# Kernel optimization log

Measured on AMD Instinct MI355X. Metric: run time of the kernel, lower is better.

## Reference

```python
import jax, jax.numpy as jnp
import numpy as np

N = 100000
E = 1600000
D_IN = 128
HID = 128
LN_EPS = 1e-5
GIN_EPS = 0.0  # PyG GINConv default eps


def setup_inputs() -> dict:
    key = jax.random.key(0)
    ks = jax.random.split(key, 8)
    x = jax.random.normal(ks[0], (N, D_IN), dtype=jnp.float32)
    edge_index = jax.random.randint(ks[1], (2, E), 0, N, dtype=jnp.int64)
    s1 = 1.0 / np.sqrt(D_IN)
    s2 = 1.0 / np.sqrt(HID)
    W1 = jax.random.uniform(ks[2], (D_IN, HID), jnp.float32, -s1, s1)
    b1 = jnp.zeros((HID,), jnp.float32)
    W2 = jax.random.uniform(ks[3], (HID, HID), jnp.float32, -s2, s2)
    b2 = jnp.zeros((HID,), jnp.float32)
    gamma = jnp.ones((HID,), jnp.float32)
    beta = jnp.zeros((HID,), jnp.float32)
    Wres = jax.random.uniform(ks[4], (D_IN, HID), jnp.float32, -s1, s1)
    bres = jnp.zeros((HID,), jnp.float32)
    return {"x": x, "edge_index": edge_index, "W1": W1, "b1": b1,
            "W2": W2, "b2": b2, "gamma": gamma, "beta": beta,
            "Wres": Wres, "bres": bres}


def reference(x, edge_index, W1, b1, W2, b2, gamma, beta, Wres, bres):
    src, dst = edge_index[0], edge_index[1]
    # GIN sum aggregation: scatter-add source features onto targets. [N, D_IN]
    agg = jax.ops.segment_sum(x[src], dst, num_segments=N)
    h = (1.0 + GIN_EPS) * x + agg
    # GIN MLP: Linear -> ReLU -> Linear
    h = jax.nn.relu(h @ W1 + b1) @ W2 + b2
    # LayerNorm over hidden dim
    mu = jnp.mean(h, axis=-1, keepdims=True)
    var = jnp.mean(jnp.square(h - mu), axis=-1, keepdims=True)
    h = (h - mu) * jax.lax.rsqrt(var + LN_EPS) * gamma + beta
    # dropout p=0 is identity; residual linear path
    return h + (x @ Wres + bres)
```

## Files before the change

### kernel.cpp

```cpp
#include <hip/hip_runtime.h>

#define NN 100000
#define NE 1600000
#define D 128
#define RT 64
#define NB 196
#define CAP 9216
#define PADB 136
#define TS 16
#define CVB 2048
#define BKB 391

typedef unsigned short u16;
typedef __attribute__((ext_vector_type(8))) short bf16x8;
typedef __attribute__((ext_vector_type(4))) float f32x4;

__device__ __forceinline__ u16 f2bf(float f) {
  unsigned int u = __float_as_uint(f);
  u += 0x7fffu + ((u >> 16) & 1u);
  return (u16)(u >> 16);
}

__global__ __launch_bounds__(256) void prep_convert(
    const float* __restrict__ x,
    const float* __restrict__ W1, const float* __restrict__ W2,
    const float* __restrict__ Wres,
    u16* __restrict__ xh, u16* __restrict__ wt) {
  int b = blockIdx.x;
  int t = threadIdx.x;
  if (b < CVB) {
    for (int q = b * 256 + t; q < 3200000; q += CVB * 256) {
      float4 v = ((const float4*)x)[q];
      uint2 pk;
      pk.x = (unsigned)f2bf(v.x) | ((unsigned)f2bf(v.y) << 16);
      pk.y = (unsigned)f2bf(v.z) | ((unsigned)f2bf(v.w) << 16);
      ((uint2*)xh)[q] = pk;
    }
  } else {
    const float* W = (b == CVB) ? Wres : (b == CVB + 1) ? W1 : W2;
    u16* dst = wt + (size_t)(b - CVB) * 16384;
    for (int i = t; i < 16384; i += 256) {
      int n = i >> 7, k = i & 127;
      dst[i] = f2bf(W[k * 128 + n]);
    }
  }
}

__global__ __launch_bounds__(256) void bucket_kernel(const int* __restrict__ ei,
                                                     int* __restrict__ tail,
                                                     unsigned* __restrict__ buf) {
  __shared__ int lhist[NB], lbase[NB];
  int t = threadIdx.x;
  size_t e0 = (size_t)blockIdx.x * 4096;
  int s_[16], d_[16];
  for (int j = t; j < NB; j += 256) lhist[j] = 0;
  __syncthreads();
#pragma unroll
  for (int k = 0; k < 16; ++k) {
    size_t e = e0 + t + (size_t)k * 256;
    if (e < NE) {
      d_[k] = ei[NE + e];
      s_[k] = ei[e];
      atomicAdd(&lhist[d_[k] >> 9], 1);
    } else {
      d_[k] = -1;
    }
  }
  __syncthreads();
  for (int j = t; j < NB; j += 256) {
    int c = lhist[j];
    lbase[j] = c ? atomicAdd(&tail[j * TS], c) : 0;
    lhist[j] = 0;
  }
  __syncthreads();
#pragma unroll
  for (int k = 0; k < 16; ++k) {
    if (d_[k] >= 0) {
      int bk = d_[k] >> 9;
      int r = lbase[bk] + atomicAdd(&lhist[bk], 1);
      if (r < CAP)
        buf[(size_t)bk * CAP + r] = (unsigned)s_[k] | ((unsigned)(d_[k] & 511) << 17);
    }
  }
}

__global__ __launch_bounds__(512) void build_csr(const unsigned* __restrict__ buf,
                                                 const int* __restrict__ tail,
                                                 int* __restrict__ cnt,
                                                 int* __restrict__ start,
                                                 int* __restrict__ csr) {
  __shared__ int lhist[512], lpre[512], lsum[64];
  int b = blockIdx.x, t = threadIdx.x;
  int nE = tail[b * TS];
  if (nE > CAP) nE = CAP;
  size_t bBase = (size_t)b * CAP;
  lhist[t] = 0;
  __syncthreads();
  for (int i = t; i < nE; i += 512)
    atomicAdd(&lhist[buf[bBase + i] >> 17], 1);
  __syncthreads();
  if (t < 64) {
    int s = 0;
#pragma unroll
    for (int k = 0; k < 8; ++k) { int v = lhist[t * 8 + k]; lpre[t * 8 + k] = s; s += v; }
    lsum[t] = s;
  }
  __syncthreads();
  if (t == 0) {
    int s = 0;
    for (int k = 0; k < 64; ++k) { int v = lsum[k]; lsum[k] = s; s += v; }
  }
  __syncthreads();
  if (t < 64) {
    int o = lsum[t];
#pragma unroll
    for (int k = 0; k < 8; ++k) lpre[t * 8 + k] += o;
  }
  __syncthreads();
  int node = (b << 9) + t;
  if (node < NN) {
    cnt[node] = lhist[t];
    start[node] = (int)bBase + lpre[t];
  }
  lhist[t] = 0;
  __syncthreads();
  for (int i = t; i < nE; i += 512) {
    unsigned e = buf[bBase + i];
    int dl = e >> 17;
    int r = atomicAdd(&lhist[dl], 1);
    csr[bBase + lpre[dl] + r] = (int)(e & 0x1FFFFu);
  }
}

#define BFACC8(aL, aH, v)                                  \
  { aL.x += __uint_as_float((v).x << 16);                  \
    aL.y += __uint_as_float((v).x & 0xffff0000u);          \
    aL.z += __uint_as_float((v).y << 16);                  \
    aL.w += __uint_as_float((v).y & 0xffff0000u);          \
    aH.x += __uint_as_float((v).z << 16);                  \
    aH.y += __uint_as_float((v).z & 0xffff0000u);          \
    aH.z += __uint_as_float((v).w << 16);                  \
    aH.w += __uint_as_float((v).w & 0xffff0000u); }

__global__ __launch_bounds__(256, 6) void gather_kernel(const float* __restrict__ x,
                                                        const u16* __restrict__ xh,
                                                        const int* __restrict__ cnt,
                                                        const int* __restrict__ start,
                                                        const int* __restrict__ csr,
                                                        u16* __restrict__ h0h) {
  int g = blockIdx.x * 16 + (threadIdx.x >> 4);
  if (g >= NN) return;
  int lane = threadIdx.x & 15;
  int fo = lane * 8;
  int n = cnt[g];
  const int* sp = csr + start[g];

  float4 aL0 = make_float4(0.f, 0.f, 0.f, 0.f);
  float4 aH0 = aL0, aL1 = aL0, aH1 = aL0;

  int nfull = n & ~3;
  if (nfull > 0) {
    int s0 = sp[0], s1 = sp[1], s2 = sp[2], s3 = sp[3];
    uint4 v0 = *(const uint4*)&xh[(size_t)s0 * D + fo];
    uint4 v1 = *(const uint4*)&xh[(size_t)s1 * D + fo];
    uint4 v2 = *(const uint4*)&xh[(size_t)s2 * D + fo];
    uint4 v3 = *(const uint4*)&xh[(size_t)s3 * D + fo];
#pragma unroll 2
    for (int j = 4; j < nfull; j += 4) {
      int t0 = sp[j], t1 = sp[j + 1], t2 = sp[j + 2], t3 = sp[j + 3];
      uint4 w0 = *(const uint4*)&xh[(size_t)t0 * D + fo];
      uint4 w1 = *(const uint4*)&xh[(size_t)t1 * D + fo];
      uint4 w2 = *(const uint4*)&xh[(size_t)t2 * D + fo];
      uint4 w3 = *(const uint4*)&xh[(size_t)t3 * D + fo];
      BFACC8(aL0, aH0, v0); BFACC8(aL1, aH1, v1);
      BFACC8(aL0, aH0, v2); BFACC8(aL1, aH1, v3);
      v0 = w0; v1 = w1; v2 = w2; v3 = w3;
    }
    BFACC8(aL0, aH0, v0); BFACC8(aL1, aH1, v1);
    BFACC8(aL0, aH0, v2); BFACC8(aL1, aH1, v3);
  }
  for (int j = nfull; j < n; ++j) {
    uint4 v0 = *(const uint4*)&xh[(size_t)sp[j] * D + fo];
    BFACC8(aL0, aH0, v0);
  }

  const float* xp = &x[(size_t)g * D + fo];
  float4 x0 = *(const float4*)xp;
  float4 x1 = *(const float4*)(xp + 4);
  float h0 = x0.x + aL0.x + aL1.x;
  float h1 = x0.y + aL0.y + aL1.y;
  float h2 = x0.z + aL0.z + aL1.z;
  float h3 = x0.w + aL0.w + aL1.w;
  float h4 = x1.x + aH0.x + aH1.x;
  float h5 = x1.y + aH0.y + aH1.y;
  float h6 = x1.z + aH0.z + aH1.z;
  float h7 = x1.w + aH0.w + aH1.w;
  uint4 pk;
  pk.x = (unsigned)f2bf(h0) | ((unsigned)f2bf(h1) << 16);
  pk.y = (unsigned)f2bf(h2) | ((unsigned)f2bf(h3) << 16);
  pk.z = (unsigned)f2bf(h4) | ((unsigned)f2bf(h5) << 16);
  pk.w = (unsigned)f2bf(h6) | ((unsigned)f2bf(h7) << 16);
  *(uint4*)&h0h[(size_t)g * 256 + fo] = pk;
}

__global__ __launch_bounds__(256, 3) void fused_kernel(
    const u16* __restrict__ xh, const u16* __restrict__ h0h,
    const u16* __restrict__ wt,
    const float* __restrict__ b1, const float* __restrict__ b2,
    const float* __restrict__ gamma, const float* __restrict__ beta,
    const float* __restrict__ bres, float* __restrict__ out) {
  __shared__ u16 Ws[128 * PADB];
  __shared__ u16 Hs[RT * PADB];

  const int t = threadIdx.x;
  const int w = t >> 6;
  const int lane = t & 63;
  const int quad = lane >> 4;
  const int l16 = lane & 15;
  const int row0 = blockIdx.x * RT;

  auto stageW = [&](const u16* __restrict__ src) {
#pragma unroll
    for (int i = 0; i < 16; ++i) {
      int v = t + i * 256;
      int r = v >> 5;
      int c4 = (v & 31) << 2;
      *(uint2*)&Ws[r * PADB + c4] = *(const uint2*)&src[r * D + c4];
    }
  };

  f32x4 acc[8], accR[8];
  f32x4 zz = {0.f, 0.f, 0.f, 0.f};
#pragma unroll
  for (int i = 0; i < 8; ++i) { acc[i] = zz; accR[i] = zz; }

  auto gemmGA = [&](const u16* __restrict__ Ag, int astride, f32x4 (&dd)[8]) {
    bf16x8 af[4];
    int ar = row0 + w * 16 + l16;
    if (ar > NN - 1) ar = NN - 1;
#pragma unroll
    for (int s = 0; s < 4; ++s)
      af[s] = *(const bf16x8*)&Ag[(size_t)ar * astride + s * 32 + quad * 8];
#pragma unroll
    for (int nt = 0; nt < 8; ++nt) {
      const u16* wp = &Ws[(nt * 16 + l16) * PADB + quad * 8];
#pragma unroll
      for (int s = 0; s < 4; ++s) {
        bf16x8 bf = *(const bf16x8*)&wp[s * 32];
        dd[nt] = __builtin_amdgcn_mfma_f32_16x16x32_bf16(af[s], bf, dd[nt], 0, 0, 0);
      }
    }
  };
  auto gemmLA = [&](f32x4 (&dd)[8]) {
    bf16x8 af[4];
#pragma unroll
    for (int s = 0; s < 4; ++s)
      af[s] = *(const bf16x8*)&Hs[(w * 16 + l16) * PADB + s * 32 + quad * 8];
#pragma unroll
    for (int nt = 0; nt < 8; ++nt) {
      const u16* wp = &Ws[(nt * 16 + l16) * PADB + quad * 8];
#pragma unroll
      for (int s = 0; s < 4; ++s) {
        bf16x8 bf = *(const bf16x8*)&wp[s * 32];
        dd[nt] = __builtin_amdgcn_mfma_f32_16x16x32_bf16(af[s], bf, dd[nt], 0, 0, 0);
      }
    }
  };

  stageW(wt);
  __syncthreads();
  gemmGA(xh, D, accR);
  __syncthreads();
  stageW(wt + 16384);
  __syncthreads();
  gemmGA(h0h, 256, acc);
  __syncthreads();

#pragma unroll
  for (int nt = 0; nt < 8; ++nt) {
    int col = nt * 16 + l16;
    float bb = b1[col];
#pragma unroll
    for (int r = 0; r < 4; ++r) {
      float hv = acc[nt][r] + bb;
      hv = hv > 0.f ? hv : 0.f;
      Hs[(w * 16 + quad * 4 + r) * PADB + col] = f2bf(hv);
      acc[nt][r] = 0.f;
    }
  }
  stageW(wt + 32768);
  __syncthreads();
  gemmLA(acc);

  float b2v[8], gv[8], bev[8], brv[8];
#pragma unroll
  for (int nt = 0; nt < 8; ++nt) {
    int col = nt * 16 + l16;
    b2v[nt] = b2[col];
    gv[nt] = gamma[col];
    bev[nt] = beta[col];
    brv[nt] = bres[col];
  }
#pragma unroll
  for (int r = 0; r < 4; ++r) {
    float s = 0.f, s2 = 0.f;
#pragma unroll
    for (int nt = 0; nt < 8; ++nt) {
      float h = acc[nt][r] + b2v[nt];
      s += h;
      s2 += h * h;
    }
    for (int m = 1; m <= 8; m <<= 1) {
      s += __shfl_xor(s, m);
      s2 += __shfl_xor(s2, m);
    }
    float mu = s * 0.0078125f;
    float var = s2 * 0.0078125f - mu * mu;
    float rs = rsqrtf(var + 1e-5f);
    int row = row0 + w * 16 + quad * 4 + r;
    if (row < NN) {
#pragma unroll
      for (int nt = 0; nt < 8; ++nt) {
        float h = acc[nt][r] + b2v[nt];
        out[(size_t)row * D + nt * 16 + l16] =
            (h - mu) * rs * gv[nt] + bev[nt] + accR[nt][r] + brv[nt];
      }
    }
  }
}

extern "C" void kernel_launch(void* const* d_in, const int* in_sizes, int n_in,
                              void* d_out, int out_size, void* d_ws, size_t ws_size,
                              hipStream_t stream) {
  const float* x     = (const float*)d_in[0];
  const int*   ei    = (const int*)d_in[1];
  const float* W1    = (const float*)d_in[2];
  const float* b1    = (const float*)d_in[3];
  const float* W2    = (const float*)d_in[4];
  const float* b2    = (const float*)d_in[5];
  const float* gamma = (const float*)d_in[6];
  const float* beta  = (const float*)d_in[7];
  const float* Wres  = (const float*)d_in[8];
  const float* bres  = (const float*)d_in[9];
  float* out = (float*)d_out;

  int*      tail  = (int*)d_ws;
  unsigned* buf   = (unsigned*)(tail + NB * TS);
  int*      cnt   = (int*)(buf + (size_t)NB * CAP);
  int*      start = cnt + NN;
  int*      csr   = start + NN;
  u16*      xh    = (u16*)(csr + (size_t)NB * CAP);
  u16*      wt    = xh + (size_t)NN * D;

  u16* h0h = (u16*)out;

  hipMemsetAsync(tail, 0, NB * TS * sizeof(int), stream);
  prep_convert<<<CVB + 3, 256, 0, stream>>>(x, W1, W2, Wres, xh, wt);
  bucket_kernel<<<BKB, 256, 0, stream>>>(ei, tail, buf);
  build_csr<<<NB, 512, 0, stream>>>(buf, tail, cnt, start, csr);
  gather_kernel<<<(NN + 15) / 16, 256, 0, stream>>>(x, xh, cnt, start, csr, h0h);
  fused_kernel<<<(NN + RT - 1) / RT, 256, 0, stream>>>(
      xh, h0h, wt, b1, b2, gamma, beta, bres, out);
}
```

Before: 257.9 us.

## Fuse neighbor gather into fused GEMM kernel, staging aggregated rows in LDS

Removes the separate gather kernel and performs the CSR neighbor aggregation inside the fused MLP kernel, writing the bf16 h0 tile directly into shared memory instead of a global scratch buffer. This eliminates a kernel launch and the global write/read of the aggregated feature matrix. The Wres weight staging is issued before the gather to overlap with it. The risk is that the latency-bound random gather now runs at the lower occupancy of the LDS-heavy GEMM kernel.

```diff
diff --git a/kernel.cpp b/kernel.cpp
--- a/kernel.cpp
+++ b/kernel.cpp
@@ -142,70 +142,10 @@
     aH.z += __uint_as_float((v).w << 16);                  \
     aH.w += __uint_as_float((v).w & 0xffff0000u); }
 
-__global__ __launch_bounds__(256, 6) void gather_kernel(const float* __restrict__ x,
-                                                        const u16* __restrict__ xh,
-                                                        const int* __restrict__ cnt,
-                                                        const int* __restrict__ start,
-                                                        const int* __restrict__ csr,
-                                                        u16* __restrict__ h0h) {
-  int g = blockIdx.x * 16 + (threadIdx.x >> 4);
-  if (g >= NN) return;
-  int lane = threadIdx.x & 15;
-  int fo = lane * 8;
-  int n = cnt[g];
-  const int* sp = csr + start[g];
-
-  float4 aL0 = make_float4(0.f, 0.f, 0.f, 0.f);
-  float4 aH0 = aL0, aL1 = aL0, aH1 = aL0;
-
-  int nfull = n & ~3;
-  if (nfull > 0) {
-    int s0 = sp[0], s1 = sp[1], s2 = sp[2], s3 = sp[3];
-    uint4 v0 = *(const uint4*)&xh[(size_t)s0 * D + fo];
-    uint4 v1 = *(const uint4*)&xh[(size_t)s1 * D + fo];
-    uint4 v2 = *(const uint4*)&xh[(size_t)s2 * D + fo];
-    uint4 v3 = *(const uint4*)&xh[(size_t)s3 * D + fo];
-#pragma unroll 2
-    for (int j = 4; j < nfull; j += 4) {
-      int t0 = sp[j], t1 = sp[j + 1], t2 = sp[j + 2], t3 = sp[j + 3];
-      uint4 w0 = *(const uint4*)&xh[(size_t)t0 * D + fo];
-      uint4 w1 = *(const uint4*)&xh[(size_t)t1 * D + fo];
-      uint4 w2 = *(const uint4*)&xh[(size_t)t2 * D + fo];
-      uint4 w3 = *(const uint4*)&xh[(size_t)t3 * D + fo];
-      BFACC8(aL0, aH0, v0); BFACC8(aL1, aH1, v1);
-      BFACC8(aL0, aH0, v2); BFACC8(aL1, aH1, v3);
-      v0 = w0; v1 = w1; v2 = w2; v3 = w3;
-    }
-    BFACC8(aL0, aH0, v0); BFACC8(aL1, aH1, v1);
-    BFACC8(aL0, aH0, v2); BFACC8(aL1, aH1, v3);
-  }
-  for (int j = nfull; j < n; ++j) {
-    uint4 v0 = *(const uint4*)&xh[(size_t)sp[j] * D + fo];
-    BFACC8(aL0, aH0, v0);
-  }
-
-  const float* xp = &x[(size_t)g * D + fo];
-  float4 x0 = *(const float4*)xp;
-  float4 x1 = *(const float4*)(xp + 4);
-  float h0 = x0.x + aL0.x + aL1.x;
-  float h1 = x0.y + aL0.y + aL1.y;
-  float h2 = x0.z + aL0.z + aL1.z;
-  float h3 = x0.w + aL0.w + aL1.w;
-  float h4 = x1.x + aH0.x + aH1.x;
-  float h5 = x1.y + aH0.y + aH1.y;
-  float h6 = x1.z + aH0.z + aH1.z;
-  float h7 = x1.w + aH0.w + aH1.w;
-  uint4 pk;
-  pk.x = (unsigned)f2bf(h0) | ((unsigned)f2bf(h1) << 16);
-  pk.y = (unsigned)f2bf(h2) | ((unsigned)f2bf(h3) << 16);
-  pk.z = (unsigned)f2bf(h4) | ((unsigned)f2bf(h5) << 16);
-  pk.w = (unsigned)f2bf(h6) | ((unsigned)f2bf(h7) << 16);
-  *(uint4*)&h0h[(size_t)g * 256 + fo] = pk;
-}
-
 __global__ __launch_bounds__(256, 3) void fused_kernel(
-    const u16* __restrict__ xh, const u16* __restrict__ h0h,
-    const u16* __restrict__ wt,
+    const float* __restrict__ x, const u16* __restrict__ xh,
+    const int* __restrict__ cnt, const int* __restrict__ start,
+    const int* __restrict__ csr, const u16* __restrict__ wt,
     const float* __restrict__ b1, const float* __restrict__ b2,
     const float* __restrict__ gamma, const float* __restrict__ beta,
     const float* __restrict__ bres, float* __restrict__ out) {
@@ -229,18 +169,78 @@
     }
   };
 
+  stageW(wt);
+
+  {
+    const int grp = t >> 4;
+    const int gl = t & 15;
+    const int fo = gl * 8;
+    for (int pass = 0; pass < 4; ++pass) {
+      int r = pass * 16 + grp;
+      int g = row0 + r;
+      uint4 pk = make_uint4(0u, 0u, 0u, 0u);
+      if (g < NN) {
+        int n = cnt[g];
+        const int* sp = csr + start[g];
+        float4 aL0 = make_float4(0.f, 0.f, 0.f, 0.f);
+        float4 aH0 = aL0, aL1 = aL0, aH1 = aL0;
+        int nfull = n & ~3;
+        if (nfull > 0) {
+          int s0 = sp[0], s1 = sp[1], s2 = sp[2], s3 = sp[3];
+          uint4 v0 = *(const uint4*)&xh[(size_t)s0 * D + fo];
+          uint4 v1 = *(const uint4*)&xh[(size_t)s1 * D + fo];
+          uint4 v2 = *(const uint4*)&xh[(size_t)s2 * D + fo];
+          uint4 v3 = *(const uint4*)&xh[(size_t)s3 * D + fo];
+#pragma unroll 2
+          for (int j = 4; j < nfull; j += 4) {
+            int t0 = sp[j], t1 = sp[j + 1], t2 = sp[j + 2], t3 = sp[j + 3];
+            uint4 w0 = *(const uint4*)&xh[(size_t)t0 * D + fo];
+            uint4 w1 = *(const uint4*)&xh[(size_t)t1 * D + fo];
+            uint4 w2 = *(const uint4*)&xh[(size_t)t2 * D + fo];
+            uint4 w3 = *(const uint4*)&xh[(size_t)t3 * D + fo];
+            BFACC8(aL0, aH0, v0); BFACC8(aL1, aH1, v1);
+            BFACC8(aL0, aH0, v2); BFACC8(aL1, aH1, v3);
+            v0 = w0; v1 = w1; v2 = w2; v3 = w3;
+          }
+          BFACC8(aL0, aH0, v0); BFACC8(aL1, aH1, v1);
+          BFACC8(aL0, aH0, v2); BFACC8(aL1, aH1, v3);
+        }
+        for (int j = nfull; j < n; ++j) {
+          uint4 v0 = *(const uint4*)&xh[(size_t)sp[j] * D + fo];
+          BFACC8(aL0, aH0, v0);
+        }
+        const float* xp = &x[(size_t)g * D + fo];
+        float4 x0 = *(const float4*)xp;
+        float4 x1 = *(const float4*)(xp + 4);
+        float h0 = x0.x + aL0.x + aL1.x;
+        float h1 = x0.y + aL0.y + aL1.y;
+        float h2 = x0.z + aL0.z + aL1.z;
+        float h3 = x0.w + aL0.w + aL1.w;
+        float h4 = x1.x + aH0.x + aH1.x;
+        float h5 = x1.y + aH0.y + aH1.y;
+        float h6 = x1.z + aH0.z + aH1.z;
+        float h7 = x1.w + aH0.w + aH1.w;
+        pk.x = (unsigned)f2bf(h0) | ((unsigned)f2bf(h1) << 16);
+        pk.y = (unsigned)f2bf(h2) | ((unsigned)f2bf(h3) << 16);
+        pk.z = (unsigned)f2bf(h4) | ((unsigned)f2bf(h5) << 16);
+        pk.w = (unsigned)f2bf(h6) | ((unsigned)f2bf(h7) << 16);
+      }
+      *(uint4*)&Hs[r * PADB + fo] = pk;
+    }
+  }
+
   f32x4 acc[8], accR[8];
   f32x4 zz = {0.f, 0.f, 0.f, 0.f};
 #pragma unroll
   for (int i = 0; i < 8; ++i) { acc[i] = zz; accR[i] = zz; }
 
-  auto gemmGA = [&](const u16* __restrict__ Ag, int astride, f32x4 (&dd)[8]) {
+  auto gemmGA = [&](f32x4 (&dd)[8]) {
     bf16x8 af[4];
     int ar = row0 + w * 16 + l16;
     if (ar > NN - 1) ar = NN - 1;
 #pragma unroll
     for (int s = 0; s < 4; ++s)
-      af[s] = *(const bf16x8*)&Ag[(size_t)ar * astride + s * 32 + quad * 8];
+      af[s] = *(const bf16x8*)&xh[(size_t)ar * D + s * 32 + quad * 8];
 #pragma unroll
     for (int nt = 0; nt < 8; ++nt) {
       const u16* wp = &Ws[(nt * 16 + l16) * PADB + quad * 8];
@@ -267,13 +267,12 @@
     }
   };
 
-  stageW(wt);
-  __syncthreads();
-  gemmGA(xh, D, accR);
+  __syncthreads();
+  gemmGA(accR);
   __syncthreads();
   stageW(wt + 16384);
   __syncthreads();
-  gemmGA(h0h, 256, acc);
+  gemmLA(acc);
   __syncthreads();
 
 #pragma unroll
@@ -352,13 +351,10 @@
   u16*      xh    = (u16*)(csr + (size_t)NB * CAP);
   u16*      wt    = xh + (size_t)NN * D;
 
-  u16* h0h = (u16*)out;
-
   hipMemsetAsync(tail, 0, NB * TS * sizeof(int), stream);
   prep_convert<<<CVB + 3, 256, 0, stream>>>(x, W1, W2, Wres, xh, wt);
   bucket_kernel<<<BKB, 256, 0, stream>>>(ei, tail, buf);
   build_csr<<<NB, 512, 0, stream>>>(buf, tail, cnt, start, csr);
-  gather_kernel<<<(NN + 15) / 16, 256, 0, stream>>>(x, xh, cnt, start, csr, h0h);
   fused_kernel<<<(NN + RT - 1) / RT, 256, 0, stream>>>(
-      xh, h0h, wt, b1, b2, gamma, beta, bres, out);
-}
+      x, xh, cnt, start, csr, wt, b1, b2, gamma, beta, bres, out);
+}
```

Measured after the change: 268.8 us. +4.2%, slower.
